# Kernel tuning notes

Hardware: AMD Instinct MI355X
Metric: run time of the kernel (lower is better)

The kernel has to match this reference:

```python
import jax, jax.numpy as jnp
import numpy as np

EPS_NORM = 1e-12
EPS_ENT = 1e-12
TEMPERATURE = 0.5
CONTRAST_DENOM = 128.0 * 100.0


def _l2_normalize(x, axis=-1):
    n = jnp.linalg.norm(x, axis=axis, keepdims=True)
    return x / jnp.maximum(n, EPS_NORM)


def setup_inputs() -> dict:
    key0 = jax.random.key(0)
    k1, k2, k3, k4 = jax.random.split(key0, 4)
    B, L, C = 16, 2048, 512
    M = 512
    return {
        "key": jax.random.normal(k1, (B, L, C), dtype=jnp.float32),
        "query": jax.random.normal(k2, (B, L, C), dtype=jnp.float32),
        "keys": jax.random.uniform(k3, (M, C), dtype=jnp.float32),
        "values": jax.random.uniform(k4, (M, C), dtype=jnp.float32),
        "mode": 0,
    }


def reference(key, query, keys, values, mode):
    B, L, C = key.shape
    k = _l2_normalize(key.reshape(-1, C))    # [T, C]
    q = _l2_normalize(query.reshape(-1, C))  # [T, C]

    # --- gatheringLoss ---
    score = jnp.einsum('tc,mc->tm', k, keys)            # [T, M]
    # top-1 of softmax(score) == argmax(score) (softmax is monotone)
    idx = jnp.argmax(score, axis=1)                     # [T]
    nearest_values = values[idx]                        # [T, C]
    gathering_loss = jnp.mean((q - nearest_values) ** 2)

    logits = score / TEMPERATURE                        # [T, M]
    logp = jax.nn.log_softmax(logits, axis=-1)
    gathered = jnp.take_along_axis(logp, idx[:, None], axis=1)  # [T, 1]
    contrast_loss = jnp.sum(gathered) / (-CONTRAST_DENOM)

    # --- read ---
    weights = jax.nn.softmax(score, axis=-1)            # [T, M]
    # EntropyLoss: mean over rows of -sum(w * log(w + eps))
    entropy_loss = jnp.mean(-jnp.sum(weights * jnp.log(weights + EPS_ENT), axis=-1))
    read_query = weights @ values                       # [T, C]

    return (read_query.reshape(B, L, C), entropy_loss, gathering_loss,
            contrast_loss, keys, values)
```

## Files before the change

### kernel.cpp

```cpp
#include <hip/hip_runtime.h>

typedef short short8 __attribute__((ext_vector_type(8)));
typedef float floatx4 __attribute__((ext_vector_type(4)));

#define C_DIM 512
#define KQ_STRIDE 1040
#define ROWS 128

__device__ __forceinline__ unsigned short f2bf(float f) {
    unsigned u = __builtin_bit_cast(unsigned, f);
    u = u + 0x7fffu + ((u >> 16) & 1u);
    return (unsigned short)(u >> 16);
}

__device__ __forceinline__ unsigned skey(float s, int col) {
    unsigned u = __builtin_bit_cast(unsigned, s);
    u = ((int)u < 0) ? ~u : (u | 0x80000000u);
    return (u & ~0x1FFu) | (unsigned)(511 - col);
}

template <int CTRL>
__device__ __forceinline__ float dppAddF(float x) {
    int t = __builtin_amdgcn_update_dpp(0, __builtin_bit_cast(int, x), CTRL, 0xF, 0xF, true);
    return x + __builtin_bit_cast(float, t);
}
template <int CTRL>
__device__ __forceinline__ unsigned dppMaxU(unsigned x) {
    unsigned u = (unsigned)__builtin_amdgcn_update_dpp(0, (int)x, CTRL, 0xF, 0xF, true);
    return u > x ? u : x;
}
__device__ __forceinline__ float rowAdd16(float x) {
    x = dppAddF<0xB1>(x);
    x = dppAddF<0x4E>(x);
    x = dppAddF<0x124>(x);
    x = dppAddF<0x128>(x);
    return x;
}

__global__ __launch_bounds__(256) void pack_kernel(
    const float* __restrict__ keys, const float* __restrict__ values,
    unsigned short* __restrict__ keysFrag, unsigned short* __restrict__ valsFrag,
    float* __restrict__ keysOut, float* __restrict__ valsOut,
    float* __restrict__ scal) {
    int tid = blockIdx.x * 256 + threadIdx.x;
    if (tid < 65536) {
        int e  = tid & 32767;
        int l  = e & 63;
        int NT = (e >> 6) & 31;
        int kt = e >> 11;
        int li = l & 15, q4 = l >> 4;
        unsigned short tmp[8];
        if (tid < 32768) {
            const float* s = keys + (size_t)(NT * 16 + li) * C_DIM + kt * 32 + q4 * 8;
#pragma unroll
            for (int j = 0; j < 8; j++) tmp[j] = f2bf(s[j]);
            unsigned short* d = keysFrag + ((size_t)(kt * 32 + NT) * 64 + l) * 8;
            *(ushort4*)d       = make_ushort4(tmp[0], tmp[1], tmp[2], tmp[3]);
            *(ushort4*)(d + 4) = make_ushort4(tmp[4], tmp[5], tmp[6], tmp[7]);
        } else {
#pragma unroll
            for (int j = 0; j < 8; j++)
                tmp[j] = f2bf(values[(size_t)(kt * 32 + q4 * 8 + j) * C_DIM + NT * 16 + li]);
            unsigned short* d = valsFrag + ((size_t)(kt * 32 + NT) * 64 + l) * 8;
            *(ushort4*)d       = make_ushort4(tmp[0], tmp[1], tmp[2], tmp[3]);
            *(ushort4*)(d + 4) = make_ushort4(tmp[4], tmp[5], tmp[6], tmp[7]);
        }
    } else {
        int ct = tid - 65536;
        if (ct == 0) { scal[0] = 0.f; scal[1] = 0.f; scal[2] = 0.f; }
#pragma unroll
        for (int i = 0; i < 4; i++) {
            int idx = ct + i * 32768;
            if (idx < 65536) ((float4*)keysOut)[idx] = ((const float4*)keys)[idx];
            else             ((float4*)valsOut)[idx - 65536] = ((const float4*)values)[idx - 65536];
        }
    }
}

__global__ __launch_bounds__(512, 2) void score_kernel(
    const float* __restrict__ key,
    const unsigned short* __restrict__ keysFrag,
    float* __restrict__ outRQ,
    float* __restrict__ scal) {
    __shared__ char kq[ROWS * KQ_STRIDE];
    __shared__ __align__(16) float stats[8][ROWS][4];

    const int tid = threadIdx.x;
    const int w  = tid >> 6;
    const int l  = tid & 63;
    const int li = l & 15;
    const int q4 = l >> 4;
    const int row0 = blockIdx.x << 7;
    char* outb = (char*)outRQ;

#pragma unroll
    for (int it = 0; it < 4; it++) {
        int r = (w << 4) + (it << 2) + q4;
        const float4* src = (const float4*)(key + (size_t)(row0 + r) * C_DIM);
        float4 v[8];
        float ss = 0.f;
#pragma unroll
        for (int i = 0; i < 8; i++) {
            v[i] = src[i * 16 + li];
            ss += v[i].x * v[i].x + v[i].y * v[i].y + v[i].z * v[i].z + v[i].w * v[i].w;
        }
        ss = rowAdd16(ss);
        float inv = 1.0f / fmaxf(sqrtf(ss), 1e-12f);
        char* dstrow = kq + r * KQ_STRIDE;
#pragma unroll
        for (int i = 0; i < 8; i++) {
            ushort4 b = make_ushort4(f2bf(v[i].x * inv), f2bf(v[i].y * inv),
                                     f2bf(v[i].z * inv), f2bf(v[i].w * inv));
            *(ushort4*)(dstrow + i * 128 + li * 8) = b;
        }
    }
    __syncthreads();

    floatx4 acc1[32];
#pragma unroll
    for (int i = 0; i < 32; i++) acc1[i] = (floatx4){0.f, 0.f, 0.f, 0.f};
    {
        const short8* kf = (const short8*)keysFrag;
        short8 bcur[4], bnxt[4];
#pragma unroll
        for (int nt = 0; nt < 4; nt++) bcur[nt] = kf[(size_t)((w * 4 + nt) * 64 + l)];
        for (int kt = 0; kt < 16; kt++) {
            if (kt < 15) {
#pragma unroll
                for (int nt = 0; nt < 4; nt++)
                    bnxt[nt] = kf[(size_t)(((kt + 1) * 32 + w * 4 + nt) * 64 + l)];
            }
            short8 a[8];
#pragma unroll
            for (int rg = 0; rg < 8; rg++)
                a[rg] = *(const short8*)(kq + (rg * 16 + li) * KQ_STRIDE + kt * 64 + q4 * 16);
#pragma unroll
            for (int rg = 0; rg < 8; rg++)
#pragma unroll
                for (int nt = 0; nt < 4; nt++)
                    acc1[rg * 4 + nt] = __builtin_amdgcn_mfma_f32_16x16x32_bf16(
                        a[rg], bcur[nt], acc1[rg * 4 + nt], 0, 0, 0);
#pragma unroll
            for (int nt = 0; nt < 4; nt++) bcur[nt] = bnxt[nt];
        }
    }

#pragma unroll
    for (int rg = 0; rg < 8; rg++) {
#pragma unroll
        for (int reg = 0; reg < 4; reg++) {
            const int colbase = (w << 6) + li;
            float s0 = acc1[rg * 4 + 0][reg];
            float s1 = acc1[rg * 4 + 1][reg];
            float s2 = acc1[rg * 4 + 2][reg];
            float s3 = acc1[rg * 4 + 3][reg];
            unsigned K  = skey(s0, colbase);
            unsigned K1 = skey(s1, colbase + 16);
            unsigned K2 = skey(s2, colbase + 32);
            unsigned K3 = skey(s3, colbase + 48);
            K = K1 > K ? K1 : K;
            K = K2 > K ? K2 : K;
            K = K3 > K ? K3 : K;
            float p0 = __expf(s0), p1 = __expf(s1), p2 = __expf(s2), p3 = __expf(s3);
            float z1 = (p0 + p1) + (p2 + p3);
            float e1 = p0 * s0 + p1 * s1 + p2 * s2 + p3 * s3;
            float z2 = p0 * p0 + p1 * p1 + p2 * p2 + p3 * p3;
            acc1[rg * 4 + 0][reg] = p0;
            acc1[rg * 4 + 1][reg] = p1;
            acc1[rg * 4 + 2][reg] = p2;
            acc1[rg * 4 + 3][reg] = p3;
            K = dppMaxU<0xB1>(K);  z1 = dppAddF<0xB1>(z1);  e1 = dppAddF<0xB1>(e1);  z2 = dppAddF<0xB1>(z2);
            K = dppMaxU<0x4E>(K);  z1 = dppAddF<0x4E>(z1);  e1 = dppAddF<0x4E>(e1);  z2 = dppAddF<0x4E>(z2);
            K = dppMaxU<0x124>(K); z1 = dppAddF<0x124>(z1); e1 = dppAddF<0x124>(e1); z2 = dppAddF<0x124>(z2);
            K = dppMaxU<0x128>(K); z1 = dppAddF<0x128>(z1); e1 = dppAddF<0x128>(e1); z2 = dppAddF<0x128>(z2);
            if (li == 0) {
                floatx4 sv;
                sv[0] = __builtin_bit_cast(float, K);
                sv[1] = z1; sv[2] = e1; sv[3] = z2;
                *(floatx4*)stats[w][rg * 16 + q4 * 4 + reg] = sv;
            }
        }
    }
    __syncthreads();

    if (w == 0) {
        unsigned KA, KB; float z1A, e1A, z2A, z1B, e1B, z2B;
        floatx4 vA = *(const floatx4*)stats[0][l];
        floatx4 vB = *(const floatx4*)stats[0][64 + l];
        KA = __builtin_bit_cast(unsigned, vA[0]); z1A = vA[1]; e1A = vA[2]; z2A = vA[3];
        KB = __builtin_bit_cast(unsigned, vB[0]); z1B = vB[1]; e1B = vB[2]; z2B = vB[3];
#pragma unroll
        for (int p = 1; p < 8; p++) {
            floatx4 uA = *(const floatx4*)stats[p][l];
            floatx4 uB = *(const floatx4*)stats[p][64 + l];
            unsigned KoA = __builtin_bit_cast(unsigned, uA[0]);
            unsigned KoB = __builtin_bit_cast(unsigned, uB[0]);
            KA = KoA > KA ? KoA : KA; z1A += uA[1]; e1A += uA[2]; z2A += uA[3];
            KB = KoB > KB ? KoB : KB; z1B += uB[1]; e1B += uB[2]; z2B += uB[3];
        }
        float izA = 1.0f / z1A, izB = 1.0f / z1B;
        int idxA = 511 - (int)(KA & 0x1FFu);
        int idxB = 511 - (int)(KB & 0x1FFu);
        char* h0 = outb + (size_t)(row0 + l) * 2048;
        char* h1 = outb + (size_t)(row0 + 64 + l) * 2048;
        *(float*)h0 = izA; *(int*)(h0 + 4) = idxA;
        *(float*)h1 = izB; *(int*)(h1 + 4) = idxB;
        unsigned umA = (KA >> 31) ? (KA & 0x7FFFFFFFu) : ~KA;
        unsigned umB = (KB >> 31) ? (KB & 0x7FFFFFFFu) : ~KB;
        umA &= ~0x1FFu; umB &= ~0x1FFu;
        float m1A = __builtin_bit_cast(float, umA);
        float m1B = __builtin_bit_cast(float, umB);
        float ent = (__logf(z1A) - e1A * izA) + (__logf(z1B) - e1B * izB);
        float con = (__logf(z2A) - 2.0f * m1A) + (__logf(z2B) - 2.0f * m1B);
#pragma unroll
        for (int msk = 1; msk < 64; msk <<= 1) {
            ent += __shfl_xor(ent, msk, 64);
            con += __shfl_xor(con, msk, 64);
        }
        if (l == 0) {
            atomicAdd(&scal[0], ent * (1.0f / 32768.0f));
            atomicAdd(&scal[2], con * (1.0f / 12800.0f));
        }
    }

#pragma unroll
    for (int rg = 0; rg < 8; rg++) {
#pragma unroll
        for (int reg = 0; reg < 4; reg++) {
            int r = rg * 16 + q4 * 4 + reg;
#pragma unroll
            for (int nt = 0; nt < 4; nt++) {
                int col = (w << 6) + nt * 16 + li;
                *(unsigned short*)(kq + r * KQ_STRIDE + col * 2) = f2bf(acc1[rg * 4 + nt][reg]);
            }
        }
    }
    __syncthreads();

#pragma unroll
    for (int it = 0; it < 16; it++) {
        int r = (w << 4) + it;
        float4 t = *(const float4*)(kq + r * KQ_STRIDE + l * 16);
        *(float4*)(outb + (size_t)(row0 + r) * 2048 + 1024 + l * 16) = t;
    }
}

__global__ __launch_bounds__(256) void gather_kernel(
    const float* __restrict__ query,
    const float* __restrict__ values,
    const float* __restrict__ outRQ,
    float* __restrict__ scal) {
    __shared__ float gpart[4];
    const int tid = threadIdx.x;
    const int w = tid >> 6;
    const int l = tid & 63;
    const char* outb = (const char*)outRQ;
    const int row0 = blockIdx.x * 32;

    float gacc = 0.f;
#pragma unroll
    for (int rr = 0; rr < 8; rr++) {
        int r = row0 + w * 8 + rr;
        int idxr = *(const int*)(outb + (size_t)r * 2048 + 4);
        const float4* qr = (const float4*)(query + (size_t)r * C_DIM);
        float4 a = qr[l * 2], b = qr[l * 2 + 1];
        float ss = a.x * a.x + a.y * a.y + a.z * a.z + a.w * a.w +
                   b.x * b.x + b.y * b.y + b.z * b.z + b.w * b.w;
        ss = rowAdd16(ss);
        ss += __shfl_xor(ss, 16, 64);
        ss += __shfl_xor(ss, 32, 64);
        float inv = 1.0f / fmaxf(sqrtf(ss), 1e-12f);
        const float4* vr = (const float4*)(values + (size_t)idxr * C_DIM);
        float4 va = vr[l * 2], vb = vr[l * 2 + 1];
        float d;
        d = a.x * inv - va.x; gacc += d * d;
        d = a.y * inv - va.y; gacc += d * d;
        d = a.z * inv - va.z; gacc += d * d;
        d = a.w * inv - va.w; gacc += d * d;
        d = b.x * inv - vb.x; gacc += d * d;
        d = b.y * inv - vb.y; gacc += d * d;
        d = b.z * inv - vb.z; gacc += d * d;
        d = b.w * inv - vb.w; gacc += d * d;
    }
    gacc = rowAdd16(gacc);
    gacc += __shfl_xor(gacc, 16, 64);
    gacc += __shfl_xor(gacc, 32, 64);
    if (l == 0) gpart[w] = gacc;
    __syncthreads();
    if (tid == 0) {
        float s = gpart[0] + gpart[1] + gpart[2] + gpart[3];
        atomicAdd(&scal[1], s * (1.0f / (32768.0f * 512.0f)));
    }
}

__global__ __launch_bounds__(512, 2) void pv_kernel(
    const unsigned short* __restrict__ valsFrag,
    float* __restrict__ outRQ) {
    __shared__ char kq[ROWS * KQ_STRIDE];
    __shared__ float izsh[ROWS];

    const int tid = threadIdx.x;
    const int w  = tid >> 6;
    const int l  = tid & 63;
    const int li = l & 15;
    const int q4 = l >> 4;
    const int row0 = blockIdx.x << 7;
    char* outb = (char*)outRQ;

    if (tid < ROWS) izsh[tid] = *(const float*)(outb + (size_t)(row0 + tid) * 2048);
#pragma unroll
    for (int it = 0; it < 16; it++) {
        int r = (w << 4) + it;
        float4 t = *(const float4*)(outb + (size_t)(row0 + r) * 2048 + 1024 + l * 16);
        *(float4*)(kq + r * KQ_STRIDE + l * 16) = t;
    }
    __syncthreads();

    floatx4 acc2[32];
#pragma unroll
    for (int i = 0; i < 32; i++) acc2[i] = (floatx4){0.f, 0.f, 0.f, 0.f};
    {
        const short8* vf = (const short8*)valsFrag;
        short8 bcur[4], bnxt[4];
#pragma unroll
        for (int nt = 0; nt < 4; nt++) bcur[nt] = vf[(size_t)((w * 4 + nt) * 64 + l)];
        for (int kt = 0; kt < 16; kt++) {
            if (kt < 15) {
#pragma unroll
                for (int nt = 0; nt < 4; nt++)
                    bnxt[nt] = vf[(size_t)(((kt + 1) * 32 + w * 4 + nt) * 64 + l)];
            }
            short8 a[8];
#pragma unroll
            for (int rg = 0; rg < 8; rg++)
                a[rg] = *(const short8*)(kq + (rg * 16 + li) * KQ_STRIDE + kt * 64 + q4 * 16);
#pragma unroll
            for (int rg = 0; rg < 8; rg++)
#pragma unroll
                for (int nt = 0; nt < 4; nt++)
                    acc2[rg * 4 + nt] = __builtin_amdgcn_mfma_f32_16x16x32_bf16(
                        a[rg], bcur[nt], acc2[rg * 4 + nt], 0, 0, 0);
#pragma unroll
            for (int nt = 0; nt < 4; nt++) bcur[nt] = bnxt[nt];
        }
    }

#pragma unroll
    for (int rg = 0; rg < 8; rg++) {
#pragma unroll
        for (int reg = 0; reg < 4; reg++) {
            int r = rg * 16 + q4 * 4 + reg;
            float izr = izsh[r];
            float* orow = outRQ + (size_t)(row0 + r) * C_DIM + (w << 6) + li;
#pragma unroll
            for (int nt = 0; nt < 4; nt++) orow[nt * 16] = acc2[rg * 4 + nt][reg] * izr;
        }
    }
}

extern "C" void kernel_launch(void* const* d_in, const int* in_sizes, int n_in,
                              void* d_out, int out_size, void* d_ws, size_t ws_size,
                              hipStream_t stream) {
    (void)in_sizes; (void)n_in; (void)out_size; (void)ws_size;
    const float* key    = (const float*)d_in[0];
    const float* query  = (const float*)d_in[1];
    const float* keysIn = (const float*)d_in[2];
    const float* valsIn = (const float*)d_in[3];
    float* out = (float*)d_out;

    unsigned short* keysFrag = (unsigned short*)d_ws;
    unsigned short* valsFrag = keysFrag + 512 * 512;

    float* outRQ   = out;
    float* scal    = out + 16777216;
    float* keysOut = out + 16777219;
    float* valsOut = keysOut + 262144;

    pack_kernel<<<384, 256, 0, stream>>>(keysIn, valsIn, keysFrag, valsFrag,
                                         keysOut, valsOut, scal);
    score_kernel<<<256, 512, 0, stream>>>(key, keysFrag, outRQ, scal);
    gather_kernel<<<1024, 256, 0, stream>>>(query, valsIn, outRQ, scal);
    pv_kernel<<<256, 512, 0, stream>>>(valsFrag, outRQ);
}
```

Before: 234.8 us.

## Halve score tile rows and stream K-chunks with deferred normalization

The score kernel now processes 64 rows per block instead of 128, and launches 512 blocks with a higher occupancy hint. Key rows are streamed in 8 column chunks, and each chunk is written to LDS as bf16 just before its MFMA steps. The L2 normalization is applied afterwards as a per-row scale on the scores. The PV kernel likewise streams its probability tile into LDS chunk by chunk inside the MFMA loop rather than loading it all up front. The aim is to overlap global loads with matrix math and improve occupancy, at the cost of more barriers and of bf16-rounding the unnormalized keys, which changes numerics slightly.

Result: slower. 242.2 us (+3.2%).

```diff
diff --git a/kernel.cpp b/kernel.cpp
--- a/kernel.cpp
+++ b/kernel.cpp
@@ -5,6 +5,7 @@
 
 #define C_DIM 512
 #define KQ_STRIDE 1040
+#define SROWS 64
 #define ROWS 128
 
 __device__ __forceinline__ unsigned short f2bf(float f) {
@@ -77,83 +78,88 @@
     }
 }
 
-__global__ __launch_bounds__(512, 2) void score_kernel(
+__global__ __launch_bounds__(512, 4) void score_kernel(
     const float* __restrict__ key,
     const unsigned short* __restrict__ keysFrag,
     float* __restrict__ outRQ,
     float* __restrict__ scal) {
-    __shared__ char kq[ROWS * KQ_STRIDE];
-    __shared__ __align__(16) float stats[8][ROWS][4];
+    __shared__ char kq[SROWS * KQ_STRIDE];
+    __shared__ __align__(16) float stats[8][SROWS][4];
+    __shared__ float invsh[SROWS];
 
     const int tid = threadIdx.x;
     const int w  = tid >> 6;
     const int l  = tid & 63;
     const int li = l & 15;
     const int q4 = l >> 4;
-    const int row0 = blockIdx.x << 7;
+    const int row0 = blockIdx.x << 6;
     char* outb = (char*)outRQ;
 
-#pragma unroll
-    for (int it = 0; it < 4; it++) {
-        int r = (w << 4) + (it << 2) + q4;
-        const float4* src = (const float4*)(key + (size_t)(row0 + r) * C_DIM);
-        float4 v[8];
-        float ss = 0.f;
-#pragma unroll
-        for (int i = 0; i < 8; i++) {
-            v[i] = src[i * 16 + li];
-            ss += v[i].x * v[i].x + v[i].y * v[i].y + v[i].z * v[i].z + v[i].w * v[i].w;
-        }
-        ss = rowAdd16(ss);
-        float inv = 1.0f / fmaxf(sqrtf(ss), 1e-12f);
-        char* dstrow = kq + r * KQ_STRIDE;
-#pragma unroll
-        for (int i = 0; i < 8; i++) {
-            ushort4 b = make_ushort4(f2bf(v[i].x * inv), f2bf(v[i].y * inv),
-                                     f2bf(v[i].z * inv), f2bf(v[i].w * inv));
-            *(ushort4*)(dstrow + i * 128 + li * 8) = b;
-        }
-    }
-    __syncthreads();
-
-    floatx4 acc1[32];
-#pragma unroll
-    for (int i = 0; i < 32; i++) acc1[i] = (floatx4){0.f, 0.f, 0.f, 0.f};
-    {
-        const short8* kf = (const short8*)keysFrag;
-        short8 bcur[4], bnxt[4];
-#pragma unroll
-        for (int nt = 0; nt < 4; nt++) bcur[nt] = kf[(size_t)((w * 4 + nt) * 64 + l)];
-        for (int kt = 0; kt < 16; kt++) {
+    const float4* src0 = (const float4*)(key + (size_t)(row0 + w * 8 + q4) * C_DIM);
+    const float4* src1 = (const float4*)(key + (size_t)(row0 + w * 8 + 4 + q4) * C_DIM);
+
+    floatx4 acc1[16];
+#pragma unroll
+    for (int i = 0; i < 16; i++) acc1[i] = (floatx4){0.f, 0.f, 0.f, 0.f};
+
+    const short8* kf = (const short8*)keysFrag;
+    short8 bcur[4], bnxt[4];
+#pragma unroll
+    for (int nt = 0; nt < 4; nt++) bcur[nt] = kf[(size_t)((w * 4 + nt) * 64 + l)];
+
+    float4 va0 = src0[li], va1 = src1[li];
+    float4 vb0, vb1;
+    float ss0 = 0.f, ss1 = 0.f;
+
+    for (int c = 0; c < 8; ++c) {
+        if (c < 7) { vb0 = src0[(c + 1) * 16 + li]; vb1 = src1[(c + 1) * 16 + li]; }
+        ss0 += va0.x * va0.x + va0.y * va0.y + va0.z * va0.z + va0.w * va0.w;
+        ss1 += va1.x * va1.x + va1.y * va1.y + va1.z * va1.z + va1.w * va1.w;
+        *(ushort4*)(kq + (w * 8 + q4) * KQ_STRIDE + c * 128 + li * 8) =
+            make_ushort4(f2bf(va0.x), f2bf(va0.y), f2bf(va0.z), f2bf(va0.w));
+        *(ushort4*)(kq + (w * 8 + 4 + q4) * KQ_STRIDE + c * 128 + li * 8) =
+            make_ushort4(f2bf(va1.x), f2bf(va1.y), f2bf(va1.z), f2bf(va1.w));
+        __syncthreads();
+#pragma unroll
+        for (int k2 = 0; k2 < 2; ++k2) {
+            int kt = c * 2 + k2;
             if (kt < 15) {
 #pragma unroll
                 for (int nt = 0; nt < 4; nt++)
                     bnxt[nt] = kf[(size_t)(((kt + 1) * 32 + w * 4 + nt) * 64 + l)];
             }
-            short8 a[8];
-#pragma unroll
-            for (int rg = 0; rg < 8; rg++)
-                a[rg] = *(const short8*)(kq + (rg * 16 + li) * KQ_STRIDE + kt * 64 + q4 * 16);
-#pragma unroll
-            for (int rg = 0; rg < 8; rg++)
+#pragma unroll
+            for (int rg = 0; rg < 4; ++rg) {
+                short8 a = *(const short8*)(kq + (rg * 16 + li) * KQ_STRIDE + kt * 64 + q4 * 16);
 #pragma unroll
                 for (int nt = 0; nt < 4; nt++)
                     acc1[rg * 4 + nt] = __builtin_amdgcn_mfma_f32_16x16x32_bf16(
-                        a[rg], bcur[nt], acc1[rg * 4 + nt], 0, 0, 0);
+                        a, bcur[nt], acc1[rg * 4 + nt], 0, 0, 0);
+            }
 #pragma unroll
             for (int nt = 0; nt < 4; nt++) bcur[nt] = bnxt[nt];
         }
-    }
-
-#pragma unroll
-    for (int rg = 0; rg < 8; rg++) {
+        va0 = vb0; va1 = vb1;
+    }
+
+    ss0 = rowAdd16(ss0);
+    ss1 = rowAdd16(ss1);
+    if (li == 0) {
+        invsh[w * 8 + q4]     = 1.0f / fmaxf(sqrtf(ss0), 1e-12f);
+        invsh[w * 8 + 4 + q4] = 1.0f / fmaxf(sqrtf(ss1), 1e-12f);
+    }
+    __syncthreads();
+
+#pragma unroll
+    for (int rg = 0; rg < 4; rg++) {
 #pragma unroll
         for (int reg = 0; reg < 4; reg++) {
             const int colbase = (w << 6) + li;
-            float s0 = acc1[rg * 4 + 0][reg];
-            float s1 = acc1[rg * 4 + 1][reg];
-            float s2 = acc1[rg * 4 + 2][reg];
-            float s3 = acc1[rg * 4 + 3][reg];
+            const float inv = invsh[rg * 16 + q4 * 4 + reg];
+            float s0 = acc1[rg * 4 + 0][reg] * inv;
+            float s1 = acc1[rg * 4 + 1][reg] * inv;
+            float s2 = acc1[rg * 4 + 2][reg] * inv;
+            float s3 = acc1[rg * 4 + 3][reg] * inv;
             unsigned K  = skey(s0, colbase);
             unsigned K1 = skey(s1, colbase + 16);
             unsigned K2 = skey(s2, colbase + 32);
@@ -184,34 +190,25 @@
     __syncthreads();
 
     if (w == 0) {
-        unsigned KA, KB; float z1A, e1A, z2A, z1B, e1B, z2B;
-        floatx4 vA = *(const floatx4*)stats[0][l];
-        floatx4 vB = *(const floatx4*)stats[0][64 + l];
-        KA = __builtin_bit_cast(unsigned, vA[0]); z1A = vA[1]; e1A = vA[2]; z2A = vA[3];
-        KB = __builtin_bit_cast(unsigned, vB[0]); z1B = vB[1]; e1B = vB[2]; z2B = vB[3];
+        unsigned K; float z1, e1, z2;
+        floatx4 v = *(const floatx4*)stats[0][l];
+        K = __builtin_bit_cast(unsigned, v[0]); z1 = v[1]; e1 = v[2]; z2 = v[3];
 #pragma unroll
         for (int p = 1; p < 8; p++) {
-            floatx4 uA = *(const floatx4*)stats[p][l];
-            floatx4 uB = *(const floatx4*)stats[p][64 + l];
-            unsigned KoA = __builtin_bit_cast(unsigned, uA[0]);
-            unsigned KoB = __builtin_bit_cast(unsigned, uB[0]);
-            KA = KoA > KA ? KoA : KA; z1A += uA[1]; e1A += uA[2]; z2A += uA[3];
-            KB = KoB > KB ? KoB : KB; z1B += uB[1]; e1B += uB[2]; z2B += uB[3];
-        }
-        float izA = 1.0f / z1A, izB = 1.0f / z1B;
-        int idxA = 511 - (int)(KA & 0x1FFu);
-        int idxB = 511 - (int)(KB & 0x1FFu);
-        char* h0 = outb + (size_t)(row0 + l) * 2048;
-        char* h1 = outb + (size_t)(row0 + 64 + l) * 2048;
-        *(float*)h0 = izA; *(int*)(h0 + 4) = idxA;
-        *(float*)h1 = izB; *(int*)(h1 + 4) = idxB;
-        unsigned umA = (KA >> 31) ? (KA & 0x7FFFFFFFu) : ~KA;
-        unsigned umB = (KB >> 31) ? (KB & 0x7FFFFFFFu) : ~KB;
-        umA &= ~0x1FFu; umB &= ~0x1FFu;
-        float m1A = __builtin_bit_cast(float, umA);
-        float m1B = __builtin_bit_cast(float, umB);
-        float ent = (__logf(z1A) - e1A * izA) + (__logf(z1B) - e1B * izB);
-        float con = (__logf(z2A) - 2.0f * m1A) + (__logf(z2B) - 2.0f * m1B);
+            floatx4 u = *(const floatx4*)stats[p][l];
+            unsigned Ko = __builtin_bit_cast(unsigned, u[0]);
+            K = Ko > K ? Ko : K;
+            z1 += u[1]; e1 += u[2]; z2 += u[3];
+        }
+        float iz = 1.0f / z1;
+        int idx = 511 - (int)(K & 0x1FFu);
+        char* h = outb + (size_t)(row0 + l) * 2048;
+        *(float*)h = iz; *(int*)(h + 4) = idx;
+        unsigned um = (K >> 31) ? (K & 0x7FFFFFFFu) : ~K;
+        um &= ~0x1FFu;
+        float m1 = __builtin_bit_cast(float, um);
+        float ent = __logf(z1) - e1 * iz;
+        float con = __logf(z2) - 2.0f * m1;
 #pragma unroll
         for (int msk = 1; msk < 64; msk <<= 1) {
             ent += __shfl_xor(ent, msk, 64);
@@ -222,9 +219,8 @@
             atomicAdd(&scal[2], con * (1.0f / 12800.0f));
         }
     }
-
-#pragma unroll
-    for (int rg = 0; rg < 8; rg++) {
+#pragma unroll
+    for (int rg = 0; rg < 4; rg++) {
 #pragma unroll
         for (int reg = 0; reg < 4; reg++) {
             int r = rg * 16 + q4 * 4 + reg;
@@ -238,8 +234,8 @@
     __syncthreads();
 
 #pragma unroll
-    for (int it = 0; it < 16; it++) {
-        int r = (w << 4) + it;
+    for (int it = 0; it < 8; it++) {
+        int r = (w << 3) + it;
         float4 t = *(const float4*)(kq + r * KQ_STRIDE + l * 16);
         *(float4*)(outb + (size_t)(row0 + r) * 2048 + 1024 + l * 16) = t;
     }
@@ -308,41 +304,52 @@
     char* outb = (char*)outRQ;
 
     if (tid < ROWS) izsh[tid] = *(const float*)(outb + (size_t)(row0 + tid) * 2048);
-#pragma unroll
-    for (int it = 0; it < 16; it++) {
-        int r = (w << 4) + it;
-        float4 t = *(const float4*)(outb + (size_t)(row0 + r) * 2048 + 1024 + l * 16);
-        *(float4*)(kq + r * KQ_STRIDE + l * 16) = t;
-    }
-    __syncthreads();
+
+    const int sr = tid >> 2, sq = tid & 3;
+    const char* psrc = outb + (size_t)(row0 + sr) * 2048 + 1024 + sq * 32;
+    char* pdst = kq + sr * KQ_STRIDE + sq * 32;
 
     floatx4 acc2[32];
 #pragma unroll
     for (int i = 0; i < 32; i++) acc2[i] = (floatx4){0.f, 0.f, 0.f, 0.f};
-    {
-        const short8* vf = (const short8*)valsFrag;
-        short8 bcur[4], bnxt[4];
-#pragma unroll
-        for (int nt = 0; nt < 4; nt++) bcur[nt] = vf[(size_t)((w * 4 + nt) * 64 + l)];
-        for (int kt = 0; kt < 16; kt++) {
+
+    const short8* vf = (const short8*)valsFrag;
+    short8 bcur[4], bnxt[4];
+#pragma unroll
+    for (int nt = 0; nt < 4; nt++) bcur[nt] = vf[(size_t)((w * 4 + nt) * 64 + l)];
+
+    float4 va0 = *(const float4*)(psrc);
+    float4 va1 = *(const float4*)(psrc + 16);
+    float4 vb0, vb1;
+
+    for (int c = 0; c < 8; ++c) {
+        if (c < 7) {
+            vb0 = *(const float4*)(psrc + (c + 1) * 128);
+            vb1 = *(const float4*)(psrc + (c + 1) * 128 + 16);
+        }
+        *(float4*)(pdst + c * 128)      = va0;
+        *(float4*)(pdst + c * 128 + 16) = va1;
+        __syncthreads();
+#pragma unroll
+        for (int k2 = 0; k2 < 2; ++k2) {
+            int kt = c * 2 + k2;
             if (kt < 15) {
 #pragma unroll
                 for (int nt = 0; nt < 4; nt++)
                     bnxt[nt] = vf[(size_t)(((kt + 1) * 32 + w * 4 + nt) * 64 + l)];
             }
-            short8 a[8];
-#pragma unroll
-            for (int rg = 0; rg < 8; rg++)
-                a[rg] = *(const short8*)(kq + (rg * 16 + li) * KQ_STRIDE + kt * 64 + q4 * 16);
-#pragma unroll
-            for (int rg = 0; rg < 8; rg++)
+#pragma unroll
+            for (int rg = 0; rg < 8; ++rg) {
+                short8 a = *(const short8*)(kq + (rg * 16 + li) * KQ_STRIDE + kt * 64 + q4 * 16);
 #pragma unroll
                 for (int nt = 0; nt < 4; nt++)
                     acc2[rg * 4 + nt] = __builtin_amdgcn_mfma_f32_16x16x32_bf16(
-                        a[rg], bcur[nt], acc2[rg * 4 + nt], 0, 0, 0);
+                        a, bcur[nt], acc2[rg * 4 + nt], 0, 0, 0);
+            }
 #pragma unroll
             for (int nt = 0; nt < 4; nt++) bcur[nt] = bnxt[nt];
         }
+        va0 = vb0; va1 = vb1;
     }
 
 #pragma unroll
@@ -378,7 +385,7 @@
 
     pack_kernel<<<384, 256, 0, stream>>>(keysIn, valsIn, keysFrag, valsFrag,
                                          keysOut, valsOut, scal);
-    score_kernel<<<256, 512, 0, stream>>>(key, keysFrag, outRQ, scal);
+    score_kernel<<<512, 512, 0, stream>>>(key, keysFrag, outRQ, scal);
     gather_kernel<<<1024, 256, 0, stream>>>(query, valsIn, outRQ, scal);
     pv_kernel<<<256, 512, 0, stream>>>(valsFrag, outRQ);
 }
```

## Pipeline row loading with MFMA and fuse gather loss into PV kernel

Applied to the files above, without the earlier changes.

The score kernel now loads key rows in chunks interleaved with the MFMA k-loop and stores unnormalized bf16 values. The row norm is accumulated along the way and applied to the scores afterwards, which removes the upfront load-then-sync phase. The gather kernel is folded into the PV kernel, which also streams the probability tile into shared memory chunk by chunk and prefetches query lines. This drops one launch and overlaps global loads with matrix work, at the cost of more barriers and slightly different rounding, since unnormalized values are quantized to bf16.

New measurement: 237.7 us. About the same (+1.2%).

```diff
diff --git a/kernel.cpp b/kernel.cpp
--- a/kernel.cpp
+++ b/kernel.cpp
@@ -84,6 +84,7 @@
     float* __restrict__ scal) {
     __shared__ char kq[ROWS * KQ_STRIDE];
     __shared__ __align__(16) float stats[8][ROWS][4];
+    __shared__ float invsh[ROWS];
 
     const int tid = threadIdx.x;
     const int w  = tid >> 6;
@@ -93,67 +94,79 @@
     const int row0 = blockIdx.x << 7;
     char* outb = (char*)outRQ;
 
-#pragma unroll
-    for (int it = 0; it < 4; it++) {
-        int r = (w << 4) + (it << 2) + q4;
-        const float4* src = (const float4*)(key + (size_t)(row0 + r) * C_DIM);
-        float4 v[8];
-        float ss = 0.f;
-#pragma unroll
-        for (int i = 0; i < 8; i++) {
-            v[i] = src[i * 16 + li];
-            ss += v[i].x * v[i].x + v[i].y * v[i].y + v[i].z * v[i].z + v[i].w * v[i].w;
-        }
-        ss = rowAdd16(ss);
-        float inv = 1.0f / fmaxf(sqrtf(ss), 1e-12f);
-        char* dstrow = kq + r * KQ_STRIDE;
-#pragma unroll
-        for (int i = 0; i < 8; i++) {
-            ushort4 b = make_ushort4(f2bf(v[i].x * inv), f2bf(v[i].y * inv),
-                                     f2bf(v[i].z * inv), f2bf(v[i].w * inv));
-            *(ushort4*)(dstrow + i * 128 + li * 8) = b;
-        }
-    }
-    __syncthreads();
+    const int sr = tid >> 2, sq = tid & 3;
+    const float4* krow = (const float4*)(key + (size_t)(row0 + sr) * C_DIM);
+    char* sdst = kq + sr * KQ_STRIDE + sq * 32;
 
     floatx4 acc1[32];
 #pragma unroll
     for (int i = 0; i < 32; i++) acc1[i] = (floatx4){0.f, 0.f, 0.f, 0.f};
-    {
-        const short8* kf = (const short8*)keysFrag;
-        short8 bcur[4], bnxt[4];
-#pragma unroll
-        for (int nt = 0; nt < 4; nt++) bcur[nt] = kf[(size_t)((w * 4 + nt) * 64 + l)];
-        for (int kt = 0; kt < 16; kt++) {
+
+    const short8* kf = (const short8*)keysFrag;
+    short8 bcur[4], bnxt[4];
+#pragma unroll
+    for (int nt = 0; nt < 4; nt++) bcur[nt] = kf[(size_t)((w * 4 + nt) * 64 + l)];
+
+    float4 va[4], vb[4];
+#pragma unroll
+    for (int j = 0; j < 4; j++) va[j] = krow[sq * 4 + j];
+    float ss = 0.f;
+
+    for (int c = 0; c < 8; ++c) {
+        if (c < 7) {
+#pragma unroll
+            for (int j = 0; j < 4; j++) vb[j] = krow[(c + 1) * 16 + sq * 4 + j];
+        }
+#pragma unroll
+        for (int j = 0; j < 4; j++)
+            ss += va[j].x * va[j].x + va[j].y * va[j].y + va[j].z * va[j].z + va[j].w * va[j].w;
+        *(ushort4*)(sdst + c * 128) =
+            make_ushort4(f2bf(va[0].x), f2bf(va[0].y), f2bf(va[0].z), f2bf(va[0].w));
+        *(ushort4*)(sdst + c * 128 + 8) =
+            make_ushort4(f2bf(va[1].x), f2bf(va[1].y), f2bf(va[1].z), f2bf(va[1].w));
+        *(ushort4*)(sdst + c * 128 + 16) =
+            make_ushort4(f2bf(va[2].x), f2bf(va[2].y), f2bf(va[2].z), f2bf(va[2].w));
+        *(ushort4*)(sdst + c * 128 + 24) =
+            make_ushort4(f2bf(va[3].x), f2bf(va[3].y), f2bf(va[3].z), f2bf(va[3].w));
+        __syncthreads();
+#pragma unroll
+        for (int k2 = 0; k2 < 2; ++k2) {
+            int kt = c * 2 + k2;
             if (kt < 15) {
 #pragma unroll
                 for (int nt = 0; nt < 4; nt++)
                     bnxt[nt] = kf[(size_t)(((kt + 1) * 32 + w * 4 + nt) * 64 + l)];
             }
-            short8 a[8];
-#pragma unroll
-            for (int rg = 0; rg < 8; rg++)
-                a[rg] = *(const short8*)(kq + (rg * 16 + li) * KQ_STRIDE + kt * 64 + q4 * 16);
-#pragma unroll
-            for (int rg = 0; rg < 8; rg++)
+#pragma unroll
+            for (int rg = 0; rg < 8; ++rg) {
+                short8 a = *(const short8*)(kq + (rg * 16 + li) * KQ_STRIDE + kt * 64 + q4 * 16);
 #pragma unroll
                 for (int nt = 0; nt < 4; nt++)
                     acc1[rg * 4 + nt] = __builtin_amdgcn_mfma_f32_16x16x32_bf16(
-                        a[rg], bcur[nt], acc1[rg * 4 + nt], 0, 0, 0);
+                        a, bcur[nt], acc1[rg * 4 + nt], 0, 0, 0);
+            }
 #pragma unroll
             for (int nt = 0; nt < 4; nt++) bcur[nt] = bnxt[nt];
         }
-    }
+#pragma unroll
+        for (int j = 0; j < 4; j++) va[j] = vb[j];
+    }
+
+    ss = dppAddF<0xB1>(ss);
+    ss = dppAddF<0x4E>(ss);
+    if (sq == 0) invsh[sr] = 1.0f / fmaxf(sqrtf(ss), 1e-12f);
+    __syncthreads();
 
 #pragma unroll
     for (int rg = 0; rg < 8; rg++) {
 #pragma unroll
         for (int reg = 0; reg < 4; reg++) {
             const int colbase = (w << 6) + li;
-            float s0 = acc1[rg * 4 + 0][reg];
-            float s1 = acc1[rg * 4 + 1][reg];
-            float s2 = acc1[rg * 4 + 2][reg];
-            float s3 = acc1[rg * 4 + 3][reg];
+            const float inv = invsh[rg * 16 + q4 * 4 + reg];
+            float s0 = acc1[rg * 4 + 0][reg] * inv;
+            float s1 = acc1[rg * 4 + 1][reg] * inv;
+            float s2 = acc1[rg * 4 + 2][reg] * inv;
+            float s3 = acc1[rg * 4 + 3][reg] * inv;
             unsigned K  = skey(s0, colbase);
             unsigned K1 = skey(s1, colbase + 16);
             unsigned K2 = skey(s2, colbase + 32);
@@ -245,24 +258,102 @@
     }
 }
 
-__global__ __launch_bounds__(256) void gather_kernel(
+__global__ __launch_bounds__(512, 2) void pv_kernel(
+    const unsigned short* __restrict__ valsFrag,
     const float* __restrict__ query,
     const float* __restrict__ values,
-    const float* __restrict__ outRQ,
+    float* __restrict__ outRQ,
     float* __restrict__ scal) {
-    __shared__ float gpart[4];
+    __shared__ char kq[ROWS * KQ_STRIDE];
+    __shared__ float izsh[ROWS];
+    __shared__ int   idxsh[ROWS];
+    __shared__ float gpart[8];
+
     const int tid = threadIdx.x;
-    const int w = tid >> 6;
-    const int l = tid & 63;
-    const char* outb = (const char*)outRQ;
-    const int row0 = blockIdx.x * 32;
+    const int w  = tid >> 6;
+    const int l  = tid & 63;
+    const int li = l & 15;
+    const int q4 = l >> 4;
+    const int row0 = blockIdx.x << 7;
+    char* outb = (char*)outRQ;
+
+    const float* qtb = query + (size_t)row0 * C_DIM;
+    float tch0 = qtb[(tid)        * 32];
+    float tch1 = qtb[(tid +  512) * 32];
+    float tch2 = qtb[(tid + 1024) * 32];
+    float tch3 = qtb[(tid + 1536) * 32];
+
+    if (tid < ROWS) {
+        izsh[tid]  = *(const float*)(outb + (size_t)(row0 + tid) * 2048);
+        idxsh[tid] = *(const int*)(outb + (size_t)(row0 + tid) * 2048 + 4);
+    }
+
+    const int sr = tid >> 2, sq = tid & 3;
+    const char* psrc = outb + (size_t)(row0 + sr) * 2048 + 1024 + sq * 32;
+    char* pdst = kq + sr * KQ_STRIDE + sq * 32;
+
+    floatx4 acc2[32];
+#pragma unroll
+    for (int i = 0; i < 32; i++) acc2[i] = (floatx4){0.f, 0.f, 0.f, 0.f};
+
+    const short8* vf = (const short8*)valsFrag;
+    short8 bcur[4], bnxt[4];
+#pragma unroll
+    for (int nt = 0; nt < 4; nt++) bcur[nt] = vf[(size_t)((w * 4 + nt) * 64 + l)];
+
+    float4 va0 = *(const float4*)(psrc);
+    float4 va1 = *(const float4*)(psrc + 16);
+    float4 vb0, vb1;
+
+    for (int c = 0; c < 8; ++c) {
+        if (c < 7) {
+            vb0 = *(const float4*)(psrc + (c + 1) * 128);
+            vb1 = *(const float4*)(psrc + (c + 1) * 128 + 16);
+        }
+        *(float4*)(pdst + c * 128)      = va0;
+        *(float4*)(pdst + c * 128 + 16) = va1;
+        __syncthreads();
+#pragma unroll
+        for (int k2 = 0; k2 < 2; ++k2) {
+            int kt = c * 2 + k2;
+            if (kt < 15) {
+#pragma unroll
+                for (int nt = 0; nt < 4; nt++)
+                    bnxt[nt] = vf[(size_t)(((kt + 1) * 32 + w * 4 + nt) * 64 + l)];
+            }
+#pragma unroll
+            for (int rg = 0; rg < 8; ++rg) {
+                short8 a = *(const short8*)(kq + (rg * 16 + li) * KQ_STRIDE + kt * 64 + q4 * 16);
+#pragma unroll
+                for (int nt = 0; nt < 4; nt++)
+                    acc2[rg * 4 + nt] = __builtin_amdgcn_mfma_f32_16x16x32_bf16(
+                        a, bcur[nt], acc2[rg * 4 + nt], 0, 0, 0);
+            }
+#pragma unroll
+            for (int nt = 0; nt < 4; nt++) bcur[nt] = bnxt[nt];
+        }
+        va0 = vb0; va1 = vb1;
+    }
+    asm volatile("" :: "v"(tch0), "v"(tch1), "v"(tch2), "v"(tch3));
+
+#pragma unroll
+    for (int rg = 0; rg < 8; rg++) {
+#pragma unroll
+        for (int reg = 0; reg < 4; reg++) {
+            int r = rg * 16 + q4 * 4 + reg;
+            float izr = izsh[r];
+            float* orow = outRQ + (size_t)(row0 + r) * C_DIM + (w << 6) + li;
+#pragma unroll
+            for (int nt = 0; nt < 4; nt++) orow[nt * 16] = acc2[rg * 4 + nt][reg] * izr;
+        }
+    }
 
     float gacc = 0.f;
 #pragma unroll
-    for (int rr = 0; rr < 8; rr++) {
-        int r = row0 + w * 8 + rr;
-        int idxr = *(const int*)(outb + (size_t)r * 2048 + 4);
-        const float4* qr = (const float4*)(query + (size_t)r * C_DIM);
+    for (int rr = 0; rr < 16; rr++) {
+        int r = (w << 4) + rr;
+        int idxr = idxsh[r];
+        const float4* qr = (const float4*)(query + (size_t)(row0 + r) * C_DIM);
         float4 a = qr[l * 2], b = qr[l * 2 + 1];
         float ss = a.x * a.x + a.y * a.y + a.z * a.z + a.w * a.w +
                    b.x * b.x + b.y * b.y + b.z * b.z + b.w * b.w;
@@ -288,73 +379,10 @@
     if (l == 0) gpart[w] = gacc;
     __syncthreads();
     if (tid == 0) {
-        float s = gpart[0] + gpart[1] + gpart[2] + gpart[3];
+        float s = 0.f;
+#pragma unroll
+        for (int i = 0; i < 8; i++) s += gpart[i];
         atomicAdd(&scal[1], s * (1.0f / (32768.0f * 512.0f)));
-    }
-}
-
-__global__ __launch_bounds__(512, 2) void pv_kernel(
-    const unsigned short* __restrict__ valsFrag,
-    float* __restrict__ outRQ) {
-    __shared__ char kq[ROWS * KQ_STRIDE];
-    __shared__ float izsh[ROWS];
-
-    const int tid = threadIdx.x;
-    const int w  = tid >> 6;
-    const int l  = tid & 63;
-    const int li = l & 15;
-    const int q4 = l >> 4;
-    const int row0 = blockIdx.x << 7;
-    char* outb = (char*)outRQ;
-
-    if (tid < ROWS) izsh[tid] = *(const float*)(outb + (size_t)(row0 + tid) * 2048);
-#pragma unroll
-    for (int it = 0; it < 16; it++) {
-        int r = (w << 4) + it;
-        float4 t = *(const float4*)(outb + (size_t)(row0 + r) * 2048 + 1024 + l * 16);
-        *(float4*)(kq + r * KQ_STRIDE + l * 16) = t;
-    }
-    __syncthreads();
-
-    floatx4 acc2[32];
-#pragma unroll
-    for (int i = 0; i < 32; i++) acc2[i] = (floatx4){0.f, 0.f, 0.f, 0.f};
-    {
-        const short8* vf = (const short8*)valsFrag;
-        short8 bcur[4], bnxt[4];
-#pragma unroll
-        for (int nt = 0; nt < 4; nt++) bcur[nt] = vf[(size_t)((w * 4 + nt) * 64 + l)];
-        for (int kt = 0; kt < 16; kt++) {
-            if (kt < 15) {
-#pragma unroll
-                for (int nt = 0; nt < 4; nt++)
-                    bnxt[nt] = vf[(size_t)(((kt + 1) * 32 + w * 4 + nt) * 64 + l)];
-            }
-            short8 a[8];
-#pragma unroll
-            for (int rg = 0; rg < 8; rg++)
-                a[rg] = *(const short8*)(kq + (rg * 16 + li) * KQ_STRIDE + kt * 64 + q4 * 16);
-#pragma unroll
-            for (int rg = 0; rg < 8; rg++)
-#pragma unroll
-                for (int nt = 0; nt < 4; nt++)
-                    acc2[rg * 4 + nt] = __builtin_amdgcn_mfma_f32_16x16x32_bf16(
-                        a[rg], bcur[nt], acc2[rg * 4 + nt], 0, 0, 0);
-#pragma unroll
-            for (int nt = 0; nt < 4; nt++) bcur[nt] = bnxt[nt];
-        }
-    }
-
-#pragma unroll
-    for (int rg = 0; rg < 8; rg++) {
-#pragma unroll
-        for (int reg = 0; reg < 4; reg++) {
-            int r = rg * 16 + q4 * 4 + reg;
-            float izr = izsh[r];
-            float* orow = outRQ + (size_t)(row0 + r) * C_DIM + (w << 6) + li;
-#pragma unroll
-            for (int nt = 0; nt < 4; nt++) orow[nt * 16] = acc2[rg * 4 + nt][reg] * izr;
-        }
     }
 }
 
@@ -379,6 +407,5 @@
     pack_kernel<<<384, 256, 0, stream>>>(keysIn, valsIn, keysFrag, valsFrag,
                                          keysOut, valsOut, scal);
     score_kernel<<<256, 512, 0, stream>>>(key, keysFrag, outRQ, scal);
-    gather_kernel<<<1024, 256, 0, stream>>>(query, valsIn, outRQ, scal);
-    pv_kernel<<<256, 512, 0, stream>>>(valsFrag, outRQ);
-}
+    pv_kernel<<<256, 512, 0, stream>>>(valsFrag, query, valsIn, outRQ, scal);
+}
```
